# Kernel optimization log

Hardware: AMD Instinct MI355X
Metric: run time of the kernel (lower is better)

The kernel has to match this reference:

```python
import jax, jax.numpy as jnp
import numpy as np
import math

N = 256  # channels == model dim M
B, H, W = 8, 48, 48
EPS = 1e-5


def _kaiming(key, shape, a=math.sqrt(5)):
    # kaiming_normal_ with fan_in = shape[1] (2D weight), leaky_relu gain
    fan_in = shape[1]
    gain = math.sqrt(2.0 / (1.0 + a * a))
    std = gain / math.sqrt(fan_in)
    return std * jax.random.normal(key, shape, dtype=jnp.float32)


def setup_inputs() -> dict:
    key = jax.random.key(0)
    ks = jax.random.split(key, 6)
    x_l = jax.random.normal(ks[0], (B, N, H, W), dtype=jnp.float32)
    x_r = jax.random.normal(ks[1], (B, N, H, W), dtype=jnp.float32)
    Wq = _kaiming(ks[2], (N, N))
    Wk = _kaiming(ks[3], (N, N))
    Wv = _kaiming(ks[4], (N, N))
    Wo = _kaiming(ks[5], (N, N))
    g1 = jnp.ones((N,), jnp.float32); b1 = jnp.zeros((N,), jnp.float32)
    g2 = jnp.ones((N,), jnp.float32); b2 = jnp.zeros((N,), jnp.float32)
    return {"x_l": x_l, "x_r": x_r, "Wq": Wq, "Wk": Wk, "Wv": Wv, "Wo": Wo,
            "g1": g1, "b1": b1, "g2": g2, "b2": b2}


def _layernorm(x, g, b):
    mu = jnp.mean(x, axis=-1, keepdims=True)
    var = jnp.mean(jnp.square(x - mu), axis=-1, keepdims=True)
    return (x - mu) * jax.lax.rsqrt(var + EPS) * g + b


def reference(x_l, x_r, Wq, Wk, Wv, Wo, g1, b1, g2, b2):
    Bsz, C, Hh, Ww = x_l.shape
    S = Hh * Ww
    # [B, C, H, W] -> [B, S, C]
    xl = x_l.reshape(Bsz, C, S).transpose(0, 2, 1)
    xr = x_r.reshape(Bsz, C, S).transpose(0, 2, 1)
    xln_l = _layernorm(xl, g1, b1)
    xln_r = _layernorm(xr, g2, b2)
    Ql = xln_l @ Wq; Qr = xln_r @ Wq
    Kl = xln_l @ Wk; Kr = xln_r @ Wk
    Vl = xln_l @ Wv; Vr = xln_r @ Wv
    scale = 1.0 / math.sqrt(C)
    Al = jnp.einsum('bsc,btc->bst', Ql, Kr) * scale  # [B,S,S]
    Ar = jnp.einsum('bsc,btc->bst', Qr, Kl) * scale
    # NOTE: original uses nn.Softmax() with dim=None; for a 3-D tensor torch's
    # legacy _get_softmax_dim resolves to dim=0 (over batch). Faithfully replicated.
    Pl = jax.nn.softmax(Al, axis=0)
    Pr = jax.nn.softmax(Ar, axis=0)
    out_l = xl + (Pl @ Vl) @ Wo
    out_r = xr + (Pr @ Vr) @ Wo
    out_l = out_l.transpose(0, 2, 1).reshape(Bsz, C, Hh, Ww)
    out_r = out_r.transpose(0, 2, 1).reshape(Bsz, C, Hh, Ww)
    return out_l, out_r
```

## Files before the change

kernel.cpp:

```cpp
#include <hip/hip_runtime.h>
#include <stdint.h>

#define SDIM 2304
#define CDIM 256
#define NB   8
#define MTOT (NB * SDIM)

typedef __attribute__((ext_vector_type(8))) short short8;
typedef __attribute__((ext_vector_type(4))) float f32x4;

__device__ __forceinline__ float b2f(unsigned short h) {
  union { unsigned int u; float f; } v; v.u = ((unsigned int)h) << 16; return v.f;
}
__device__ __forceinline__ unsigned short f2b(float f) {
  union { unsigned int u; float f; } v; v.f = f;
  unsigned int u = v.u;
  u += 0x7fffu + ((u >> 16) & 1u);
  return (unsigned short)(u >> 16);
}
static inline unsigned short f2b_host(float f) {
  union { unsigned int u; float f; } v; v.f = f;
  unsigned int u = v.u;
  u += 0x7fffu + ((u >> 16) & 1u);
  return (unsigned short)(u >> 16);
}

__device__ __forceinline__ void gload_lds16(const unsigned short* g, unsigned short* l) {
  __builtin_amdgcn_global_load_lds(
      (const __attribute__((address_space(1))) unsigned int*)g,
      (__attribute__((address_space(3))) unsigned int*)l,
      16, 0, 0);
}

__global__ __launch_bounds__(64)
void detect_dtype(const unsigned short* __restrict__ x, int* __restrict__ flag)
{
  int lane = threadIdx.x;
  int bad = 0;
  for (int i = lane; i < 1024; i += 64) {
    float v = b2f(x[i]);
    if (!(fabsf(v) < 1e20f)) bad = 1;
  }
  unsigned long long m = __ballot(bad);
  if (lane == 0) flag[0] = (m != 0ULL) ? 1 : 0;
}

constexpr int EP_PLAIN = 0, EP_QKV = 1, EP_OUT = 2, EP_ACC = 3;

template <int EP>
__global__ __launch_bounds__(256, 2)
void gemm_nt(const unsigned short* __restrict__ pA, int lda, long sAz,
             const unsigned short* __restrict__ pB, int ldb, long sBz, int zx,
             unsigned short* __restrict__ pC, int ldc, long sCz,
             unsigned short* __restrict__ pQ, unsigned short* __restrict__ pK,
             unsigned short* __restrict__ pV,
             const unsigned short* __restrict__ pX0, const unsigned short* __restrict__ pX1,
             float* __restrict__ pFacc, unsigned short* __restrict__ pBf, int accmode,
             const int* __restrict__ dflag, int Kdim)
{
  __shared__ __align__(16) unsigned short As[128 * 32];
  __shared__ __align__(16) unsigned short Bs[128 * 32];

  const int tid = threadIdx.x;
  const int z = blockIdx.z;
  const long m0 = (long)blockIdx.x * 128;
  const long n0 = (long)blockIdx.y * 128;
  const unsigned short* A  = pA + (long)z * sAz;
  const unsigned short* Bm = pB + (long)(z ^ zx) * sBz;

  const int lane = tid & 63;
  const int wave = tid >> 6;
  const int wm = (wave & 1) << 6;
  const int wn = (wave >> 1) << 6;
  const int lr = lane & 15;
  const int quad = lane >> 4;

  f32x4 acc[4][4];
#pragma unroll
  for (int i = 0; i < 4; ++i)
#pragma unroll
    for (int j = 0; j < 4; ++j) acc[i][j] = (f32x4)0.0f;

  const int e0 = tid, e1 = tid + 256;
  const int r0 = e0 >> 2, c0 = (e0 & 3) << 3;
  const int r1 = e1 >> 2, c1 = (e1 & 3) << 3;
  const unsigned short* pa0 = A  + (m0 + r0) * lda + c0;
  const unsigned short* pa1 = A  + (m0 + r1) * lda + c1;
  const unsigned short* pb0 = Bm + (n0 + r0) * ldb + c0;
  const unsigned short* pb1 = Bm + (n0 + r1) * ldb + c1;

  for (int k0 = 0; k0 < Kdim; k0 += 32) {
    __syncthreads();
    gload_lds16(pa0 + k0, &As[e0 * 8]);
    gload_lds16(pa1 + k0, &As[e1 * 8]);
    gload_lds16(pb0 + k0, &Bs[e0 * 8]);
    gload_lds16(pb1 + k0, &Bs[e1 * 8]);
    __syncthreads();

    short8 af[4], bf[4];
#pragma unroll
    for (int i = 0; i < 4; ++i) {
      af[i] = *(const short8*)&As[(wm + i * 16 + lr) * 32 + quad * 8];
      bf[i] = *(const short8*)&Bs[(wn + i * 16 + lr) * 32 + quad * 8];
    }
#pragma unroll
    for (int i = 0; i < 4; ++i)
#pragma unroll
      for (int j = 0; j < 4; ++j)
        acc[i][j] = __builtin_amdgcn_mfma_f32_16x16x32_bf16(af[i], bf[j], acc[i][j], 0, 0, 0);
  }

  if constexpr (EP == EP_PLAIN) {
    unsigned short* Cp = pC + (long)z * sCz;
#pragma unroll
    for (int i = 0; i < 4; ++i) {
      const long mb = m0 + wm + i * 16 + quad * 4;
#pragma unroll
      for (int j = 0; j < 4; ++j) {
        const long n = n0 + wn + j * 16 + lr;
#pragma unroll
        for (int r = 0; r < 4; ++r)
          Cp[(mb + r) * ldc + n] = f2b(acc[i][j][r]);
      }
    }
  } else if constexpr (EP == EP_QKV) {
    const int g  = (int)(n0 >> 8);
    const int nb = (int)(n0 & 255);
    if (g < 2) {
      unsigned short* Cp = (g == 0 ? pQ : pK) + (long)z * sCz;
#pragma unroll
      for (int i = 0; i < 4; ++i) {
        const long mb = m0 + wm + i * 16 + quad * 4;
#pragma unroll
        for (int j = 0; j < 4; ++j) {
          const int n = nb + wn + j * 16 + lr;
#pragma unroll
          for (int r = 0; r < 4; ++r)
            Cp[(mb + r) * CDIM + n] = f2b(acc[i][j][r]);
        }
      }
    } else {
      const int b = (int)(m0 / SDIM);
      const int sblk = (int)(m0 % SDIM);
      unsigned short* Vz = pV + ((long)z * NB + b) * (long)CDIM * SDIM;
#pragma unroll
      for (int i = 0; i < 4; ++i) {
        const int s = sblk + wm + i * 16 + quad * 4;
#pragma unroll
        for (int j = 0; j < 4; ++j) {
          const int c = nb + wn + j * 16 + lr;
          ushort4 pk;
          pk.x = f2b(acc[i][j][0]); pk.y = f2b(acc[i][j][1]);
          pk.z = f2b(acc[i][j][2]); pk.w = f2b(acc[i][j][3]);
          *(ushort4*)&Vz[(long)c * SDIM + s] = pk;
        }
      }
    }
  } else if constexpr (EP == EP_ACC) {
    float* Fz = pFacc + (long)z * SDIM * CDIM;
    unsigned short* Bz = pBf + (long)z * SDIM * CDIM;
#pragma unroll
    for (int i = 0; i < 4; ++i) {
      const long mb = m0 + wm + i * 16 + quad * 4;
#pragma unroll
      for (int j = 0; j < 4; ++j) {
        const long n = n0 + wn + j * 16 + lr;
#pragma unroll
        for (int r = 0; r < 4; ++r) {
          const long idx = (mb + r) * CDIM + n;
          float v = acc[i][j][r];
          if (accmode != 0) v += Fz[idx];
          if (accmode == 2) Bz[idx] = f2b(v);
          else              Fz[idx] = v;
        }
      }
    }
  } else {
    const int io32 = dflag[0];
    const int b = (int)(m0 / SDIM);
    const int sblk = (int)(m0 % SDIM);
    const unsigned short* Xraw = (z == 0 ? pX0 : pX1);
    if (io32) {
      const float* Xf = (const float*)Xraw + (long)b * CDIM * SDIM;
      float* Of = (float*)pC + (long)z * sCz + (long)b * CDIM * SDIM;
#pragma unroll
      for (int i = 0; i < 4; ++i) {
        const int s = sblk + wm + i * 16 + quad * 4;
#pragma unroll
        for (int j = 0; j < 4; ++j) {
          const int c = (int)n0 + wn + j * 16 + lr;
          const long off = (long)c * SDIM + s;
          float4 rx = *(const float4*)&Xf[off];
          float4 pk;
          pk.x = acc[i][j][0] + rx.x;
          pk.y = acc[i][j][1] + rx.y;
          pk.z = acc[i][j][2] + rx.z;
          pk.w = acc[i][j][3] + rx.w;
          *(float4*)&Of[off] = pk;
        }
      }
    } else {
      const unsigned short* X = Xraw + (long)b * CDIM * SDIM;
      unsigned short* O = pC + (long)z * sCz + (long)b * CDIM * SDIM;
#pragma unroll
      for (int i = 0; i < 4; ++i) {
        const int s = sblk + wm + i * 16 + quad * 4;
#pragma unroll
        for (int j = 0; j < 4; ++j) {
          const int c = (int)n0 + wn + j * 16 + lr;
          const long off = (long)c * SDIM + s;
          ushort4 rx = *(const ushort4*)&X[off];
          ushort4 pk;
          pk.x = f2b(acc[i][j][0] + b2f(rx.x));
          pk.y = f2b(acc[i][j][1] + b2f(rx.y));
          pk.z = f2b(acc[i][j][2] + b2f(rx.z));
          pk.w = f2b(acc[i][j][3] + b2f(rx.w));
          *(ushort4*)&O[off] = pk;
        }
      }
    }
  }
}

__global__ __launch_bounds__(256)
void wtrans(const unsigned short* __restrict__ Wq, const unsigned short* __restrict__ Wk,
            const unsigned short* __restrict__ Wv, const unsigned short* __restrict__ Wo,
            unsigned short* __restrict__ WT, const int* __restrict__ dflag)
{
  const int io32 = dflag[0];
  int idx = blockIdx.x * 256 + threadIdx.x;
  int w = idx >> 16, r = idx & 65535, n = r >> 8, k = r & 255;
  const unsigned short* W = (w == 0) ? Wq : (w == 1) ? Wk : (w == 2) ? Wv : Wo;
  float v = io32 ? ((const float*)W)[k * 256 + n] : b2f(W[k * 256 + n]);
  if (w == 0) v *= 0.0625f;
  WT[w * 65536 + n * 256 + k] = f2b(v);
}

__global__ __launch_bounds__(256)
void ln_kernel(const unsigned short* __restrict__ xl, const unsigned short* __restrict__ xr,
               const unsigned short* __restrict__ g1, const unsigned short* __restrict__ b1,
               const unsigned short* __restrict__ g2, const unsigned short* __restrict__ b2,
               unsigned short* __restrict__ XLN, const int* __restrict__ dflag)
{
  const int io32 = dflag[0];
  const int strm = blockIdx.z;
  const int b = blockIdx.y;
  const int s0 = blockIdx.x * 64;
  const unsigned short* xraw = (strm ? xr : xl);
  const float*          xf = (const float*)xraw + (long)b * CDIM * SDIM;
  const unsigned short* xh = xraw + (long)b * CDIM * SDIM;
  const unsigned short* gg = strm ? g2 : g1;
  const unsigned short* bb = strm ? b2 : b1;
  const int tid = threadIdx.x;
  const int sl = tid & 63;
  const int team = tid >> 6;

  __shared__ float red[2][4][64];
  __shared__ float muS[64], rsS[64];
  __shared__ __align__(16) unsigned short tile[64 * 258];

  float sum = 0.f, sq = 0.f;
  for (int c = team * 64; c < team * 64 + 64; ++c) {
    const long off = (long)c * SDIM + s0 + sl;
    float v = io32 ? xf[off] : b2f(xh[off]);
    sum += v; sq += v * v;
  }
  red[0][team][sl] = sum; red[1][team][sl] = sq;
  __syncthreads();
  if (tid < 64) {
    float s_ = red[0][0][tid] + red[0][1][tid] + red[0][2][tid] + red[0][3][tid];
    float q_ = red[1][0][tid] + red[1][1][tid] + red[1][2][tid] + red[1][3][tid];
    float mu = s_ * (1.0f / CDIM);
    float var = q_ * (1.0f / CDIM) - mu * mu;
    muS[tid] = mu;
    rsS[tid] = rsqrtf(var + 1e-5f);
  }
  __syncthreads();
  const float mu = muS[sl], rs = rsS[sl];
  for (int c = team * 64; c < team * 64 + 64; ++c) {
    const long off = (long)c * SDIM + s0 + sl;
    float v = io32 ? xf[off] : b2f(xh[off]);
    float gv = io32 ? ((const float*)gg)[c] : b2f(gg[c]);
    float bv = io32 ? ((const float*)bb)[c] : b2f(bb[c]);
    tile[sl * 258 + c] = f2b((v - mu) * rs * gv + bv);
  }
  __syncthreads();
  unsigned short* outp = XLN + ((long)strm * MTOT + (long)b * SDIM + s0) * CDIM;
  const ushort2* t2 = (const ushort2*)tile;
  ushort2* o2 = (ushort2*)outp;
#pragma unroll
  for (int i = 0; i < 32; ++i) {
    int idx = i * 256 + tid;
    int r = idx >> 7, c2 = idx & 127;
    o2[idx] = t2[r * 129 + c2];
  }
}

__global__ __launch_bounds__(256)
void softmax_bdim(unsigned short* __restrict__ Ab, long total)
{
  const int strm = blockIdx.y;
  const long i8 = (((long)blockIdx.x << 8) + threadIdx.x) << 3;
  unsigned short* base = Ab + (long)strm * NB * total + i8;
  float v[NB][8];
#pragma unroll
  for (int b = 0; b < NB; ++b) {
    const ushort4* p = (const ushort4*)(base + (long)b * total);
    ushort4 a0 = p[0], a1 = p[1];
    v[b][0] = b2f(a0.x); v[b][1] = b2f(a0.y); v[b][2] = b2f(a0.z); v[b][3] = b2f(a0.w);
    v[b][4] = b2f(a1.x); v[b][5] = b2f(a1.y); v[b][6] = b2f(a1.z); v[b][7] = b2f(a1.w);
  }
#pragma unroll
  for (int j = 0; j < 8; ++j) {
    float mx = v[0][j];
#pragma unroll
    for (int b = 1; b < NB; ++b) mx = fmaxf(mx, v[b][j]);
    float s = 0.f;
#pragma unroll
    for (int b = 0; b < NB; ++b) { float e = __expf(v[b][j] - mx); v[b][j] = e; s += e; }
    float inv = 1.0f / s;
#pragma unroll
    for (int b = 0; b < NB; ++b) v[b][j] *= inv;
  }
#pragma unroll
  for (int b = 0; b < NB; ++b) {
    ushort4 a0, a1;
    a0.x = f2b(v[b][0]); a0.y = f2b(v[b][1]); a0.z = f2b(v[b][2]); a0.w = f2b(v[b][3]);
    a1.x = f2b(v[b][4]); a1.y = f2b(v[b][5]); a1.z = f2b(v[b][6]); a1.w = f2b(v[b][7]);
    ushort4* p = (ushort4*)(base + (long)b * total);
    p[0] = a0; p[1] = a1;
  }
}

__global__ __launch_bounds__(256)
void fill_val(unsigned short* __restrict__ out, unsigned short v, int n)
{
  int i = blockIdx.x * 256 + threadIdx.x;
  if (i < n) out[i] = v;
}

extern "C" void kernel_launch(void* const* d_in, const int* in_sizes, int n_in,
                              void* d_out, int out_size, void* d_ws, size_t ws_size,
                              hipStream_t stream)
{
  const unsigned short* xl = (const unsigned short*)d_in[0];
  const unsigned short* xr = (const unsigned short*)d_in[1];
  const unsigned short* Wq = (const unsigned short*)d_in[2];
  const unsigned short* Wk = (const unsigned short*)d_in[3];
  const unsigned short* Wv = (const unsigned short*)d_in[4];
  const unsigned short* Wo = (const unsigned short*)d_in[5];
  const unsigned short* g1 = (const unsigned short*)d_in[6];
  const unsigned short* b1 = (const unsigned short*)d_in[7];
  const unsigned short* g2 = (const unsigned short*)d_in[8];
  const unsigned short* b2 = (const unsigned short*)d_in[9];
  unsigned short* out = (unsigned short*)d_out;

  const size_t need_chunk = 113770496UL + 64;
  const size_t need_full  = 227016704UL + 64;
  if (ws_size < need_chunk) {
    float wsmb = (float)(ws_size >> 20);
    unsigned short v = f2b_host(wsmb * 100.0f);
    fill_val<<<dim3((out_size + 255) / 256), 256, 0, stream>>>(out, v, out_size);
    return;
  }

  int* dFlag = (int*)((char*)d_ws + ((ws_size - 16) & ~15UL));
  detect_dtype<<<dim3(1), 64, 0, stream>>>(xl, dFlag);

  if (ws_size >= need_full) {
    unsigned short* WT  = (unsigned short*)d_ws;
    unsigned short* Qb  = WT + 262144L;
    unsigned short* Kb  = Qb + 9437184L;
    unsigned short* Vt  = Kb + 9437184L;
    unsigned short* Ab  = Vt + 9437184L;
    unsigned short* XLN = Ab;
    unsigned short* PVbf = Qb;

    wtrans<<<dim3(1024), 256, 0, stream>>>(Wq, Wk, Wv, Wo, WT, dFlag);
    ln_kernel<<<dim3(36, 8, 2), 256, 0, stream>>>(xl, xr, g1, b1, g2, b2, XLN, dFlag);

    gemm_nt<EP_QKV><<<dim3(144, 6, 2), 256, 0, stream>>>(
        XLN, CDIM, (long)MTOT * CDIM,
        WT, CDIM, 0L, 0,
        nullptr, 0, (long)MTOT * CDIM,
        Qb, Kb, Vt, nullptr, nullptr,
        nullptr, nullptr, 0, dFlag, CDIM);

    gemm_nt<EP_PLAIN><<<dim3(18, 18, 16), 256, 0, stream>>>(
        Qb, CDIM, (long)SDIM * CDIM,
        Kb, CDIM, (long)SDIM * CDIM, 8,
        Ab, SDIM, (long)SDIM * SDIM,
        nullptr, nullptr, nullptr, nullptr, nullptr,
        nullptr, nullptr, 0, dFlag, CDIM);

    softmax_bdim<<<dim3(2592, 2), 256, 0, stream>>>(Ab, (long)SDIM * SDIM);

    gemm_nt<EP_PLAIN><<<dim3(18, 2, 16), 256, 0, stream>>>(
        Ab, SDIM, (long)SDIM * SDIM,
        Vt, SDIM, (long)CDIM * SDIM, 0,
        PVbf, CDIM, (long)SDIM * CDIM,
        nullptr, nullptr, nullptr, nullptr, nullptr,
        nullptr, nullptr, 0, dFlag, SDIM);

    gemm_nt<EP_OUT><<<dim3(144, 2, 2), 256, 0, stream>>>(
        PVbf, CDIM, (long)MTOT * CDIM,
        WT + 768L * 256, CDIM, 0L, 0,
        out, 0, (long)NB * CDIM * SDIM,
        nullptr, nullptr, nullptr, xl, xr,
        nullptr, nullptr, 0, dFlag, CDIM);
    return;
  }

  unsigned short* WT  = (unsigned short*)d_ws;
  unsigned short* XLN = WT  + 1024L * 256;
  unsigned short* Abc = XLN;
  unsigned short* Qb  = XLN + 9437184L;
  unsigned short* Kb  = Qb  + 9437184L;
  unsigned short* Vt  = Kb  + 9437184L;
  float*          PVacc = (float*)(Vt + 9437184L);
  unsigned short* PVbf  = Qb;

  wtrans<<<dim3(1024), 256, 0, stream>>>(Wq, Wk, Wv, Wo, WT, dFlag);
  ln_kernel<<<dim3(36, 8, 2), 256, 0, stream>>>(xl, xr, g1, b1, g2, b2, XLN, dFlag);

  gemm_nt<EP_QKV><<<dim3(144, 6, 2), 256, 0, stream>>>(
      XLN, CDIM, (long)MTOT * CDIM,
      WT, CDIM, 0L, 0,
      nullptr, 0, (long)MTOT * CDIM,
      Qb, Kb, Vt, nullptr, nullptr,
      nullptr, nullptr, 0, dFlag, CDIM);

  for (int tc = 0; tc < 9; ++tc) {
    gemm_nt<EP_PLAIN><<<dim3(18, 2, 16), 256, 0, stream>>>(
        Qb, CDIM, (long)SDIM * CDIM,
        Kb + (long)tc * 256 * CDIM, CDIM, (long)SDIM * CDIM, 8,
        Abc, 256, (long)SDIM * 256,
        nullptr, nullptr, nullptr, nullptr, nullptr,
        nullptr, nullptr, 0, dFlag, CDIM);

    softmax_bdim<<<dim3(288, 2), 256, 0, stream>>>(Abc, (long)SDIM * 256);

    const int mode = (tc == 0) ? 0 : (tc == 8) ? 2 : 1;
    gemm_nt<EP_ACC><<<dim3(18, 2, 16), 256, 0, stream>>>(
        Abc, 256, (long)SDIM * 256,
        Vt + (long)tc * 256, SDIM, (long)CDIM * SDIM, 0,
        nullptr, 0, 0L,
        nullptr, nullptr, nullptr, nullptr, nullptr,
        PVacc, PVbf, mode, dFlag, 256);
  }

  gemm_nt<EP_OUT><<<dim3(144, 2, 2), 256, 0, stream>>>(
      PVbf, CDIM, (long)MTOT * CDIM,
      WT + 768L * 256, CDIM, 0L, 0,
      out, 0, (long)NB * CDIM * SDIM,
      nullptr, nullptr, nullptr, xl, xr,
      nullptr, nullptr, 0, dFlag, CDIM);
}
```

Before: 403.6 us.

## Fuse exp into score GEMM, split softmax normalization, fuse PV with output projection

The score GEMM now applies exp in its epilogue, which drops max subtraction from the batch-dim softmax. A small kernel computes per-position reciprocal sums across the batch. A new fused kernel multiplies probabilities by the reciprocal on load, performs P@V, then immediately applies Wo and adds the residual. This removes the separate softmax pass and the intermediate PV round-trip. Without the max shift, exp could overflow for large scores, and the normalized Ab is read twice with an extra Dr read in the PV kernel.

```diff
diff --git a/kernel.cpp b/kernel.cpp
--- a/kernel.cpp
+++ b/kernel.cpp
@@ -45,7 +45,7 @@
   if (lane == 0) flag[0] = (m != 0ULL) ? 1 : 0;
 }
 
-constexpr int EP_PLAIN = 0, EP_QKV = 1, EP_OUT = 2, EP_ACC = 3;
+constexpr int EP_PLAIN = 0, EP_QKV = 1, EP_OUT = 2, EP_ACC = 3, EP_EXP = 4;
 
 template <int EP>
 __global__ __launch_bounds__(256, 2)
@@ -110,7 +110,7 @@
         acc[i][j] = __builtin_amdgcn_mfma_f32_16x16x32_bf16(af[i], bf[j], acc[i][j], 0, 0, 0);
   }
 
-  if constexpr (EP == EP_PLAIN) {
+  if constexpr (EP == EP_PLAIN || EP == EP_EXP) {
     unsigned short* Cp = pC + (long)z * sCz;
 #pragma unroll
     for (int i = 0; i < 4; ++i) {
@@ -119,8 +119,11 @@
       for (int j = 0; j < 4; ++j) {
         const long n = n0 + wn + j * 16 + lr;
 #pragma unroll
-        for (int r = 0; r < 4; ++r)
-          Cp[(mb + r) * ldc + n] = f2b(acc[i][j][r]);
+        for (int r = 0; r < 4; ++r) {
+          float v = acc[i][j][r];
+          if constexpr (EP == EP_EXP) v = __expf(v);
+          Cp[(mb + r) * ldc + n] = f2b(v);
+        }
       }
     }
   } else if constexpr (EP == EP_QKV) {
@@ -217,6 +220,196 @@
           pk.w = f2b(acc[i][j][3] + b2f(rx.w));
           *(ushort4*)&O[off] = pk;
         }
+      }
+    }
+  }
+}
+
+__global__ __launch_bounds__(256)
+void dsum_rcp(const unsigned short* __restrict__ Ab, unsigned short* __restrict__ Dr)
+{
+  const long total = (long)SDIM * SDIM;
+  const int strm = blockIdx.y;
+  const long i8 = (((long)blockIdx.x << 8) + threadIdx.x) << 3;
+  const unsigned short* base = Ab + (long)strm * NB * total + i8;
+  float s[8] = {0.f,0.f,0.f,0.f,0.f,0.f,0.f,0.f};
+#pragma unroll
+  for (int b = 0; b < NB; ++b) {
+    short8 e = *(const short8*)(base + (long)b * total);
+#pragma unroll
+    for (int t = 0; t < 8; ++t) s[t] += b2f(((unsigned short*)&e)[t]);
+  }
+  short8 o;
+#pragma unroll
+  for (int t = 0; t < 8; ++t) ((unsigned short*)&o)[t] = f2b(1.0f / s[t]);
+  *(short8*)(Dr + (long)strm * total + i8) = o;
+}
+
+__global__ __launch_bounds__(256, 3)
+void pv_fused(const unsigned short* __restrict__ Ab,
+              const unsigned short* __restrict__ Dr,
+              const unsigned short* __restrict__ Vt,
+              const unsigned short* __restrict__ WoT,
+              const unsigned short* __restrict__ pX0,
+              const unsigned short* __restrict__ pX1,
+              unsigned short* __restrict__ outp,
+              const int* __restrict__ dflag)
+{
+  __shared__ __align__(16) unsigned short LSD[18432];
+  unsigned short* As0 = LSD;
+  unsigned short* As1 = LSD + 1024;
+  unsigned short* Bs0 = LSD + 2048;
+  unsigned short* Bs1 = LSD + 10240;
+  unsigned short* As2 = LSD;
+  unsigned short* Bs3 = LSD + 8192;
+
+  const int tid = threadIdx.x;
+  const int wave = tid >> 6;
+  const int lane = tid & 63;
+  const int lr = lane & 15;
+  const int quad = lane >> 4;
+  const int z = blockIdx.y;
+  const int strm = z >> 3;
+  const long m0 = (long)blockIdx.x * 32;
+
+  const unsigned short* Pz = Ab + (long)z * SDIM * SDIM + m0 * SDIM;
+  const unsigned short* Dz = Dr + (long)strm * SDIM * SDIM + m0 * SDIM;
+  const unsigned short* Vz = Vt + (long)z * CDIM * SDIM;
+
+  f32x4 acc[2][4];
+#pragma unroll
+  for (int i = 0; i < 2; ++i)
+#pragma unroll
+    for (int j = 0; j < 4; ++j) acc[i][j] = (f32x4)0.0f;
+
+  const int ac = tid & 127, ah = tid >> 7;
+  const int arow = ac >> 2, akc = (ac & 3) << 3;
+  const long aoff = (long)arow * SDIM + ah * 32 + akc;
+  unsigned short* AsH = ah ? As1 : As0;
+
+  for (int k0 = 0; k0 < SDIM; k0 += 64) {
+    short8 ea = *(const short8*)(Pz + aoff + k0);
+    short8 da = *(const short8*)(Dz + aoff + k0);
+    __syncthreads();
+#pragma unroll
+    for (int h = 0; h < 2; ++h) {
+      unsigned short* BsH = h ? Bs1 : Bs0;
+#pragma unroll
+      for (int q = 0; q < 4; ++q) {
+        const int cb = q * 256 + tid;
+        const int row = cb >> 2, kc = (cb & 3) << 3;
+        gload_lds16(Vz + (long)row * SDIM + k0 + h * 32 + kc, BsH + cb * 8);
+      }
+    }
+    short8 pp;
+#pragma unroll
+    for (int t = 0; t < 8; ++t)
+      ((unsigned short*)&pp)[t] =
+          f2b(b2f(((unsigned short*)&ea)[t]) * b2f(((unsigned short*)&da)[t]));
+    *(short8*)&AsH[ac * 8] = pp;
+    __syncthreads();
+
+#pragma unroll
+    for (int h = 0; h < 2; ++h) {
+      const unsigned short* Ah = h ? As1 : As0;
+      const unsigned short* Bh = h ? Bs1 : Bs0;
+      short8 af[2], bf[4];
+#pragma unroll
+      for (int i = 0; i < 2; ++i)
+        af[i] = *(const short8*)&Ah[(i * 16 + lr) * 32 + quad * 8];
+#pragma unroll
+      for (int j = 0; j < 4; ++j)
+        bf[j] = *(const short8*)&Bh[(wave * 64 + j * 16 + lr) * 32 + quad * 8];
+#pragma unroll
+      for (int i = 0; i < 2; ++i)
+#pragma unroll
+        for (int j = 0; j < 4; ++j)
+          acc[i][j] = __builtin_amdgcn_mfma_f32_16x16x32_bf16(af[i], bf[j], acc[i][j], 0, 0, 0);
+    }
+  }
+
+  __syncthreads();
+#pragma unroll
+  for (int i = 0; i < 2; ++i)
+#pragma unroll
+    for (int j = 0; j < 4; ++j) {
+      const int col = wave * 64 + j * 16 + lr;
+      const int kb = col >> 5, kin = col & 31;
+#pragma unroll
+      for (int r = 0; r < 4; ++r) {
+        const int row = i * 16 + quad * 4 + r;
+        As2[kb * 1024 + row * 32 + kin] = f2b(acc[i][j][r]);
+      }
+    }
+
+  f32x4 acc2[2][4];
+#pragma unroll
+  for (int i = 0; i < 2; ++i)
+#pragma unroll
+    for (int j = 0; j < 4; ++j) acc2[i][j] = (f32x4)0.0f;
+
+  for (int kb = 0; kb < 8; ++kb) {
+    __syncthreads();
+#pragma unroll
+    for (int q = 0; q < 4; ++q) {
+      const int cb = q * 256 + tid;
+      const int rowc = cb >> 2, kc = (cb & 3) << 3;
+      gload_lds16(WoT + (long)rowc * CDIM + kb * 32 + kc, Bs3 + cb * 8);
+    }
+    __syncthreads();
+    short8 af[2], bf[4];
+#pragma unroll
+    for (int i = 0; i < 2; ++i)
+      af[i] = *(const short8*)&As2[kb * 1024 + (i * 16 + lr) * 32 + quad * 8];
+#pragma unroll
+    for (int j = 0; j < 4; ++j)
+      bf[j] = *(const short8*)&Bs3[(wave * 64 + j * 16 + lr) * 32 + quad * 8];
+#pragma unroll
+    for (int i = 0; i < 2; ++i)
+#pragma unroll
+      for (int j = 0; j < 4; ++j)
+        acc2[i][j] = __builtin_amdgcn_mfma_f32_16x16x32_bf16(af[i], bf[j], acc2[i][j], 0, 0, 0);
+  }
+
+  const int io32 = dflag[0];
+  const int b = z & 7;
+  const unsigned short* Xraw = (strm == 0 ? pX0 : pX1);
+  if (io32) {
+    const float* Xf = (const float*)Xraw + (long)b * CDIM * SDIM;
+    float* Of = (float*)outp + (long)z * CDIM * SDIM;
+#pragma unroll
+    for (int i = 0; i < 2; ++i) {
+      const long s = m0 + i * 16 + quad * 4;
+#pragma unroll
+      for (int j = 0; j < 4; ++j) {
+        const int c = wave * 64 + j * 16 + lr;
+        const long off = (long)c * SDIM + s;
+        float4 rx = *(const float4*)&Xf[off];
+        float4 pk;
+        pk.x = acc2[i][j][0] + rx.x;
+        pk.y = acc2[i][j][1] + rx.y;
+        pk.z = acc2[i][j][2] + rx.z;
+        pk.w = acc2[i][j][3] + rx.w;
+        *(float4*)&Of[off] = pk;
+      }
+    }
+  } else {
+    const unsigned short* X = Xraw + (long)b * CDIM * SDIM;
+    unsigned short* O = outp + (long)z * CDIM * SDIM;
+#pragma unroll
+    for (int i = 0; i < 2; ++i) {
+      const long s = m0 + i * 16 + quad * 4;
+#pragma unroll
+      for (int j = 0; j < 4; ++j) {
+        const int c = wave * 64 + j * 16 + lr;
+        const long off = (long)c * SDIM + s;
+        ushort4 rx = *(const ushort4*)&X[off];
+        ushort4 pk;
+        pk.x = f2b(acc2[i][j][0] + b2f(rx.x));
+        pk.y = f2b(acc2[i][j][1] + b2f(rx.y));
+        pk.z = f2b(acc2[i][j][2] + b2f(rx.z));
+        pk.w = f2b(acc2[i][j][3] + b2f(rx.w));
+        *(ushort4*)&O[off] = pk;
       }
     }
   }
@@ -374,7 +567,7 @@
     unsigned short* Vt  = Kb + 9437184L;
     unsigned short* Ab  = Vt + 9437184L;
     unsigned short* XLN = Ab;
-    unsigned short* PVbf = Qb;
+    unsigned short* Dr  = Qb;
 
     wtrans<<<dim3(1024), 256, 0, stream>>>(Wq, Wk, Wv, Wo, WT, dFlag);
     ln_kernel<<<dim3(36, 8, 2), 256, 0, stream>>>(xl, xr, g1, b1, g2, b2, XLN, dFlag);
@@ -386,28 +579,17 @@
         Qb, Kb, Vt, nullptr, nullptr,
         nullptr, nullptr, 0, dFlag, CDIM);
 
-    gemm_nt<EP_PLAIN><<<dim3(18, 18, 16), 256, 0, stream>>>(
+    gemm_nt<EP_EXP><<<dim3(18, 18, 16), 256, 0, stream>>>(
         Qb, CDIM, (long)SDIM * CDIM,
         Kb, CDIM, (long)SDIM * CDIM, 8,
         Ab, SDIM, (long)SDIM * SDIM,
         nullptr, nullptr, nullptr, nullptr, nullptr,
         nullptr, nullptr, 0, dFlag, CDIM);
 
-    softmax_bdim<<<dim3(2592, 2), 256, 0, stream>>>(Ab, (long)SDIM * SDIM);
-
-    gemm_nt<EP_PLAIN><<<dim3(18, 2, 16), 256, 0, stream>>>(
-        Ab, SDIM, (long)SDIM * SDIM,
-        Vt, SDIM, (long)CDIM * SDIM, 0,
-        PVbf, CDIM, (long)SDIM * CDIM,
-        nullptr, nullptr, nullptr, nullptr, nullptr,
-        nullptr, nullptr, 0, dFlag, SDIM);
-
-    gemm_nt<EP_OUT><<<dim3(144, 2, 2), 256, 0, stream>>>(
-        PVbf, CDIM, (long)MTOT * CDIM,
-        WT + 768L * 256, CDIM, 0L, 0,
-        out, 0, (long)NB * CDIM * SDIM,
-        nullptr, nullptr, nullptr, xl, xr,
-        nullptr, nullptr, 0, dFlag, CDIM);
+    dsum_rcp<<<dim3(2592, 2), 256, 0, stream>>>(Ab, Dr);
+
+    pv_fused<<<dim3(72, 16), 256, 0, stream>>>(
+        Ab, Dr, Vt, WT + 768L * 256, xl, xr, out, dFlag);
     return;
   }
 
```

After: 406.1 us. Within noise of the previous version (+0.6%).
